# Kernel optimization log

Measured on AMD Instinct MI355X. Metric: run time of the kernel, lower is better.

Reference implementation:

```python
import jax, jax.numpy as jnp
import numpy as np
from jax import lax

T = 16        # in_length
E = 32        # input_embedding_size_d
H = 64        # encoder_size
NG = 32       # vehicles per scene group
G = 1024      # number of scene groups
N = G * NG    # total vehicles
C = 3         # class_num

leaky = lambda x: jax.nn.leaky_relu(x, 0.1)

def _gru_final(x_seq, Wih, Whh, bih, bhh):
    # x_seq: (T, N, E). PyTorch GRU gate order: r, z, n. Returns final hidden (N, H).
    def step(h, x):
        gx = x @ Wih.T + bih
        gh = h @ Whh.T + bhh
        xr, xz, xn = jnp.split(gx, 3, axis=-1)
        hr, hz, hn = jnp.split(gh, 3, axis=-1)
        r = jax.nn.sigmoid(xr + hr)
        z = jax.nn.sigmoid(xz + hz)
        ng = jnp.tanh(xn + r * hn)
        return (1.0 - z) * ng + z * h, None
    h0 = jnp.zeros((x_seq.shape[1], Whh.shape[1]), x_seq.dtype)
    hT, _ = lax.scan(step, h0, x_seq)
    return hT

def setup_inputs() -> dict:
    key = jax.random.key(0)
    ks = jax.random.split(key, 24)
    def rn(k, shape, fan):
        return jax.random.normal(k, shape, jnp.float32) * np.float32(1.0 / np.sqrt(fan))
    inp = {}
    inp["scene"] = jax.random.normal(ks[0], (N, 2 * T), jnp.float32)
    inp["condition"] = jax.random.randint(ks[1], (N,), 0, C, jnp.int32)
    inp["hero_pos_index"] = jax.random.randint(ks[2], (G,), 0, N, jnp.int32)
    inp["nbrs_pos_index"] = jax.random.randint(ks[3], (N,), 0, N, jnp.int32)
    inp["index_div"] = jnp.arange(N, dtype=jnp.int32).reshape(G, NG)
    # ip_emb_d: Linear(2, E)
    inp["W_emb"] = rn(ks[4], (2, E), 2)
    inp["b_emb"] = jnp.zeros((E,), jnp.float32)
    # forward / backward GRUs (weight_ih: (3H,E), weight_hh: (3H,H))
    inp["Wih_f"] = rn(ks[5], (3 * H, E), E); inp["Whh_f"] = rn(ks[6], (3 * H, H), H)
    inp["bih_f"] = jnp.zeros((3 * H,), jnp.float32); inp["bhh_f"] = jnp.zeros((3 * H,), jnp.float32)
    inp["Wih_b"] = rn(ks[7], (3 * H, E), E); inp["Whh_b"] = rn(ks[8], (3 * H, H), H)
    inp["bih_b"] = jnp.zeros((3 * H,), jnp.float32); inp["bhh_b"] = jnp.zeros((3 * H,), jnp.float32)
    # mlp: Linear(H, H//2)
    inp["Wm"] = rn(ks[9], (H, H // 2), H); inp["bm"] = jnp.zeros((H // 2,), jnp.float32)
    # spatial_mlp: Linear(2T, H) -> Linear(H, H//2)
    inp["Ws1"] = rn(ks[10], (2 * T, H), 2 * T); inp["bs1"] = jnp.zeros((H,), jnp.float32)
    inp["Ws2"] = rn(ks[11], (H, H // 2), H); inp["bs2"] = jnp.zeros((H // 2,), jnp.float32)
    # op_d: Linear(H, H//4) -> Linear(H//4, C)
    inp["Wo1"] = rn(ks[12], (H, H // 4), H); inp["bo1"] = jnp.zeros((H // 4,), jnp.float32)
    inp["Wo2"] = rn(ks[13], (H // 4, C), H // 4); inp["bo2"] = jnp.zeros((C,), jnp.float32)
    return inp

def reference(scene, condition, hero_pos_index, nbrs_pos_index, index_div,
              W_emb, b_emb, Wih_f, Whh_f, bih_f, bhh_f, Wih_b, Whh_b, bih_b, bhh_b,
              Wm, bm, Ws1, bs1, Ws2, bs2, Wo1, bo1, Wo2, bo2):
    n_total = scene.shape[0]
    # scene.view(-1,2,T).permute(2,0,1) -> (T, N, 2)
    scene_t = scene.reshape(n_total, 2, T).transpose(2, 0, 1)
    emb = leaky(scene_t @ W_emb + b_emb)                 # (T, N, E)
    h_f = _gru_final(emb, Wih_f, Whh_f, bih_f, bhh_f)    # (N, H)
    h_b = _gru_final(emb[::-1], Wih_b, Whh_b, bih_b, bhh_b)
    seq_enc = leaky(((h_f + h_b) * 0.5) @ Wm + bm)       # (N, H//2)
    # pairwise relative features within each group: rel[g, j, i] = x_i - x_j
    feat_g = scene[index_div]                            # (G, n, 2T); row layout == permute(1,2,0).view(-1,2T)
    rel = feat_g[:, None, :, :] - feat_g[:, :, None, :]  # (G, n, n, 2T)
    enc = leaky(leaky(rel @ Ws1 + bs1) @ Ws2 + bs2)      # (G, n, n, H//2)
    # diagonal pairs (i==j) are dropped in the original; subtract mlp(0) then divide by n-1
    zero_enc = leaky(leaky(bs1) @ Ws2 + bs2)             # (H//2,)
    n_grp = index_div.shape[1]
    pooled = (enc.sum(axis=2) - zero_enc) / (n_grp - 1)  # (G, n, H//2)
    pooled = pooled.reshape(n_total, -1)                 # group-concat order == vehicle order (arange groups)
    full_enc = jnp.concatenate([seq_enc, pooled], axis=1)  # (N, H)
    x_logit = leaky(full_enc @ Wo1 + bo1) @ Wo2 + bo2      # (N, C)
    return x_logit, full_enc
```

## Files before the change

### kernel.cpp

```cpp
#include <hip/hip_runtime.h>
#include <hip/hip_bf16.h>

#define TT 16
#define EE 32
#define HH 64
#define NGRP 32
#define CC 3

typedef __attribute__((ext_vector_type(8))) short short8;
typedef __attribute__((ext_vector_type(4))) short short4v;
typedef __attribute__((ext_vector_type(4))) float floatx4;

#define MFMA16(a, b, c) __builtin_amdgcn_mfma_f32_16x16x32_bf16((a), (b), (c), 0, 0, 0)

#define RLN2 1.4426950408889634f

__device__ __forceinline__ float leakyf(float x) { return fmaxf(x, 0.1f * x); }
__device__ __forceinline__ short f2bf(float x) {
    unsigned u = __float_as_uint(x);
    return (short)((u + 0x7FFFu + ((u >> 16) & 1u)) >> 16);
}
__device__ __forceinline__ short f2bf_h(float x) {
    return (short)((__float_as_uint(x) + 0x8000u) >> 16);
}
__device__ __forceinline__ float bf2f(short s) {
    return __uint_as_float(((unsigned)(unsigned short)s) << 16);
}
__device__ __forceinline__ short8 ld8bf(const float* __restrict__ p) {
    const float4 a = *(const float4*)p;
    const float4 b = *(const float4*)(p + 4);
    short8 v;
    v[0] = f2bf(a.x); v[1] = f2bf(a.y); v[2] = f2bf(a.z); v[3] = f2bf(a.w);
    v[4] = f2bf(b.x); v[5] = f2bf(b.y); v[6] = f2bf(b.z); v[7] = f2bf(b.w);
    return v;
}
__device__ __forceinline__ short8 ld8bfs(const float* __restrict__ p, float s) {
    const float4 a = *(const float4*)p;
    const float4 b = *(const float4*)(p + 4);
    short8 v;
    v[0] = f2bf(a.x * s); v[1] = f2bf(a.y * s); v[2] = f2bf(a.z * s); v[3] = f2bf(a.w * s);
    v[4] = f2bf(b.x * s); v[5] = f2bf(b.y * s); v[6] = f2bf(b.z * s); v[7] = f2bf(b.w * s);
    return v;
}

__global__ __launch_bounds__(256, 4) void gru_dir_kernel(
    const float* __restrict__ scene, const int* __restrict__ index_div,
    const float* __restrict__ W_emb, const float* __restrict__ b_emb,
    const float* __restrict__ Wih_f, const float* __restrict__ Whh_f,
    const float* __restrict__ bih_f, const float* __restrict__ bhh_f,
    const float* __restrict__ Wih_b, const float* __restrict__ Whh_b,
    const float* __restrict__ bih_b, const float* __restrict__ bhh_b,
    short* __restrict__ hws)
{
    __shared__ float sscene[32][33];
    __shared__ __align__(16) short Hf[2 * 2 * 2 * 64 * 8];
    __shared__ __align__(16) short Xb[2 * 2 * 64 * 8];

    const int bx   = blockIdx.x;
    const int g    = bx >> 1;
    const int dir  = bx & 1;
    const int tid  = threadIdx.x;
    const int lane = tid & 63;
    const int wd   = __builtin_amdgcn_readfirstlane(tid >> 6);
    const int cc   = lane & 15;
    const int quad = lane >> 4;
    const int j    = wd * 16 + cc;
    const int ks_w = j >> 5;
    const int qa_w = (j >> 3) & 3;
    const int ii_w = j & 7;

    #pragma unroll
    for (int rep = 0; rep < 4; ++rep) {
        const int idx = tid + rep * 256;
        const int v = idx >> 5, c = idx & 31;
        const int n = index_div[g * NGRP + v];
        sscene[c][v] = scene[n * 32 + c];
    }

    const float* Wih = dir ? Wih_b : Wih_f;
    const float* Whh = dir ? Whh_b : Whh_f;
    const float* bih = dir ? bih_b : bih_f;
    const float* bhh = dir ? bhh_b : bhh_f;
    const int k0 = quad * 8;
    const float SRZ = -RLN2, SN = 2.0f * RLN2;
    const short8 Br0  = ld8bfs(Whh + (j      ) * 64 + k0,      SRZ);
    const short8 Br1  = ld8bfs(Whh + (j      ) * 64 + 32 + k0, SRZ);
    const short8 Br2  = ld8bfs(Wih + (j      ) * 32 + k0,      SRZ);
    const short8 Bz0  = ld8bfs(Whh + (j +  64) * 64 + k0,      SRZ);
    const short8 Bz1  = ld8bfs(Whh + (j +  64) * 64 + 32 + k0, SRZ);
    const short8 Bz2  = ld8bfs(Wih + (j +  64) * 32 + k0,      SRZ);
    const short8 Bhn0 = ld8bfs(Whh + (j + 128) * 64 + k0,      SN);
    const short8 Bhn1 = ld8bfs(Whh + (j + 128) * 64 + 32 + k0, SN);
    const short8 Bxn  = ld8bfs(Wih + (j + 128) * 32 + k0,      SN);
    const float vb_r  = SRZ * (bih[j] + bhh[j]);
    const float vb_z  = SRZ * (bih[j + 64] + bhh[j + 64]);
    const float vb_xn = SN * bih[j + 128];
    const float vb_hn = SN * bhh[j + 128];

    const int veh_x = tid & 31;
    const int q2    = tid >> 5;
    const int e0    = q2 * 4;
    float w0e[4], w1e[4], bbe[4];
    #pragma unroll
    for (int d = 0; d < 4; ++d) {
        w0e[d] = W_emb[e0 + d];
        w1e[d] = W_emb[EE + e0 + d];
        bbe[d] = b_emb[e0 + d];
    }
    const int xoff = ((veh_x >> 4) * 64 + (q2 >> 1) * 16 + (veh_x & 15)) * 8
                   + (q2 & 1) * 4;

    __syncthreads();

    {
        const short8 z8 = {0, 0, 0, 0, 0, 0, 0, 0};
        *(short8*)&Hf[tid * 8] = z8;
        const int t0 = dir ? (TT - 1) : 0;
        const float xs = sscene[t0][veh_x];
        const float ys = sscene[16 + t0][veh_x];
        short4v v;
        #pragma unroll
        for (int d = 0; d < 4; ++d)
            v[d] = f2bf_h(leakyf(fmaf(xs, w0e[d], fmaf(ys, w1e[d], bbe[d]))));
        *(short4v*)&Xb[xoff] = v;
    }

    float h_reg[8];
    #pragma unroll
    for (int i = 0; i < 8; ++i) h_reg[i] = 0.0f;

    __syncthreads();

    #pragma unroll 2
    for (int s = 0; s < TT; ++s) {
        const int pb = s & 1, nb = pb ^ 1;
        const short* HfD = &Hf[pb * 2048];
        short*       HfN = &Hf[nb * 2048];
        const short* XbD = &Xb[pb * 1024];
        #pragma unroll
        for (int mt = 0; mt < 2; ++mt) {
            const short8 Ah0 = *(const short8*)&HfD[((0 * 2 + mt) * 64 + lane) * 8];
            const short8 Ah1 = *(const short8*)&HfD[((1 * 2 + mt) * 64 + lane) * 8];
            const short8 Axx = *(const short8*)&XbD[(mt * 64 + lane) * 8];
            const floatx4 z4 = {0.f, 0.f, 0.f, 0.f};
            const floatx4 ar  = MFMA16(Axx, Br2, MFMA16(Ah1, Br1, MFMA16(Ah0, Br0, z4)));
            const floatx4 az  = MFMA16(Axx, Bz2, MFMA16(Ah1, Bz1, MFMA16(Ah0, Bz0, z4)));
            const floatx4 ahn = MFMA16(Ah1, Bhn1, MFMA16(Ah0, Bhn0, z4));
            const floatx4 axn = MFMA16(Axx, Bxn, z4);
            #pragma unroll
            for (int r = 0; r < 4; ++r) {
                const float rr = __builtin_amdgcn_rcpf(1.0f + __builtin_amdgcn_exp2f(ar[r] + vb_r));
                const float zz = __builtin_amdgcn_rcpf(1.0f + __builtin_amdgcn_exp2f(az[r] + vb_z));
                const float y  = fmaf(rr, ahn[r] + vb_hn, axn[r] + vb_xn);
                const float ng = fmaf(-2.0f,
                                      __builtin_amdgcn_rcpf(__builtin_amdgcn_exp2f(y) + 1.0f),
                                      1.0f);
                const float h0 = h_reg[mt * 4 + r];
                h_reg[mt * 4 + r] = fmaf(zz, h0 - ng, ng);
            }
        }
        #pragma unroll
        for (int mt = 0; mt < 2; ++mt) {
            #pragma unroll
            for (int r = 0; r < 4; ++r) {
                const int slot = qa_w * 16 + quad * 4 + r;
                HfN[((ks_w * 2 + mt) * 64 + slot) * 8 + ii_w] = f2bf_h(h_reg[mt * 4 + r]);
            }
        }
        if (s + 1 < TT) {
            const int tn = dir ? (TT - 2 - s) : (s + 1);
            const float xs = sscene[tn][veh_x];
            const float ys = sscene[16 + tn][veh_x];
            short4v v;
            #pragma unroll
            for (int d = 0; d < 4; ++d)
                v[d] = f2bf_h(leakyf(fmaf(xs, w0e[d], fmaf(ys, w1e[d], bbe[d]))));
            *(short4v*)&Xb[xoff + nb * 1024] = v;
        }
        __syncthreads();
    }
    *(short8*)&hws[(size_t)bx * 2048 + tid * 8] = *(const short8*)&Hf[tid * 8];
}

__global__ __launch_bounds__(256, 4) void tail_kernel(
    const float* __restrict__ scene, const int* __restrict__ index_div,
    const short* __restrict__ hws,
    const float* __restrict__ Wm, const float* __restrict__ bm,
    const float* __restrict__ Ws1, const float* __restrict__ bs1,
    const float* __restrict__ Ws2, const float* __restrict__ bs2,
    const float* __restrict__ Wo1, const float* __restrict__ bo1,
    const float* __restrict__ Wo2, const float* __restrict__ bo2,
    float* __restrict__ full_enc, float* __restrict__ out)
{
    __shared__ float sscene[32][33];
    __shared__ float su[NGRP][68];
    __shared__ float fe[NGRP][68];
    __shared__ float swo1[1024];
    __shared__ float szero[32];

    const int g    = blockIdx.x;
    const int tid  = threadIdx.x;
    const int lane = tid & 63;
    const int w    = __builtin_amdgcn_readfirstlane(tid >> 6);
    const int cc   = lane & 15;
    const int quad = lane >> 4;

    #pragma unroll
    for (int rep = 0; rep < 4; ++rep) {
        const int idx = tid + rep * 256;
        const int v = idx >> 5, c = idx & 31;
        const int n = index_div[g * NGRP + v];
        sscene[c][v] = scene[n * 32 + c];
    }
    *(float4*)&swo1[tid * 4] = *(const float4*)&Wo1[tid * 4];
    if (tid < 32) {
        float zs = bs2[tid];
        #pragma unroll
        for (int d = 0; d < HH; ++d) zs = fmaf(leakyf(bs1[d]), Ws2[d * 32 + tid], zs);
        szero[tid] = leakyf(zs);
    }
    __syncthreads();

    {
        const int v  = tid >> 3;
        const int d0 = (tid & 7) * 8;
        float acc[8];
        #pragma unroll
        for (int i = 0; i < 8; ++i) acc[i] = 0.0f;
        #pragma unroll
        for (int e = 0; e < EE; ++e) {
            const float f = sscene[e][v];
            const float4 w0 = *(const float4*)&Ws1[e * 64 + d0];
            const float4 w1 = *(const float4*)&Ws1[e * 64 + d0 + 4];
            acc[0] = fmaf(f, w0.x, acc[0]); acc[1] = fmaf(f, w0.y, acc[1]);
            acc[2] = fmaf(f, w0.z, acc[2]); acc[3] = fmaf(f, w0.w, acc[3]);
            acc[4] = fmaf(f, w1.x, acc[4]); acc[5] = fmaf(f, w1.y, acc[5]);
            acc[6] = fmaf(f, w1.z, acc[6]); acc[7] = fmaf(f, w1.w, acc[7]);
        }
        #pragma unroll
        for (int i = 0; i < 8; ++i) su[v][d0 + i] = acc[i];
    }

    {
        const int nt   = w >> 1;
        const int mt_e = w & 1;
        const int n_col = nt * 16 + cc;
        short8 Bm0, Bm1;
        #pragma unroll
        for (int i = 0; i < 8; ++i) {
            Bm0[i] = f2bf(Wm[(     quad * 8 + i) * 32 + n_col]);
            Bm1[i] = f2bf(Wm[(32 + quad * 8 + i) * 32 + n_col]);
        }
        short8 A0, A1;
        #pragma unroll
        for (int ks = 0; ks < 2; ++ks) {
            const short8 F = *(const short8*)&hws[(size_t)(g * 2 + 0) * 2048 + ((ks * 2 + mt_e) * 64 + lane) * 8];
            const short8 B = *(const short8*)&hws[(size_t)(g * 2 + 1) * 2048 + ((ks * 2 + mt_e) * 64 + lane) * 8];
            #pragma unroll
            for (int i = 0; i < 8; ++i) {
                const short v = f2bf(0.5f * (bf2f(F[i]) + bf2f(B[i])));
                if (ks == 0) A0[i] = v; else A1[i] = v;
            }
        }
        const floatx4 z4 = {0.f, 0.f, 0.f, 0.f};
        const floatx4 acc = MFMA16(A1, Bm1, MFMA16(A0, Bm0, z4));
        const float bmn = bm[n_col];
        #pragma unroll
        for (int r = 0; r < 4; ++r) {
            const int veh = mt_e * 16 + quad * 4 + r;
            const float sv = leakyf(acc[r] + bmn);
            const int n = index_div[g * NGRP + veh];
            full_enc[n * HH + n_col] = sv;
            fe[veh][n_col] = sv;
        }
    }

    short8 Bw00, Bw01, Bw10, Bw11;
    #pragma unroll
    for (int i = 0; i < 8; ++i) {
        Bw00[i] = f2bf(Ws2[(     quad * 8 + i) * 32 + cc]);
        Bw01[i] = f2bf(Ws2[(32 + quad * 8 + i) * 32 + cc]);
        Bw10[i] = f2bf(Ws2[(     quad * 8 + i) * 32 + 16 + cc]);
        Bw11[i] = f2bf(Ws2[(32 + quad * 8 + i) * 32 + 16 + cc]);
    }
    float bsq0[8], bsq1[8];
    #pragma unroll
    for (int i = 0; i < 8; ++i) {
        bsq0[i] = bs1[quad * 8 + i];
        bsq1[i] = bs1[32 + quad * 8 + i];
    }
    const float bs2c0 = bs2[cc], bs2c1 = bs2[16 + cc];
    __syncthreads();

    #pragma unroll 2
    for (int jj = 0; jj < 8; ++jj) {
        const int jrow = w * 8 + jj;
        float vj0[8], vj1[8];
        #pragma unroll
        for (int i = 0; i < 8; ++i) {
            vj0[i] = su[jrow][quad * 8 + i] - bsq0[i];
            vj1[i] = su[jrow][32 + quad * 8 + i] - bsq1[i];
        }
        float acc0 = 0.0f, acc1 = 0.0f;
        #pragma unroll
        for (int it = 0; it < 2; ++it) {
            const int irow = it * 16 + cc;
            const float4 p0 = *(const float4*)&su[irow][quad * 8];
            const float4 p1 = *(const float4*)&su[irow][quad * 8 + 4];
            const float4 p2 = *(const float4*)&su[irow][32 + quad * 8];
            const float4 p3 = *(const float4*)&su[irow][32 + quad * 8 + 4];
            short8 A0, A1;
            A0[0] = f2bf(leakyf(p0.x - vj0[0])); A0[1] = f2bf(leakyf(p0.y - vj0[1]));
            A0[2] = f2bf(leakyf(p0.z - vj0[2])); A0[3] = f2bf(leakyf(p0.w - vj0[3]));
            A0[4] = f2bf(leakyf(p1.x - vj0[4])); A0[5] = f2bf(leakyf(p1.y - vj0[5]));
            A0[6] = f2bf(leakyf(p1.z - vj0[6])); A0[7] = f2bf(leakyf(p1.w - vj0[7]));
            A1[0] = f2bf(leakyf(p2.x - vj1[0])); A1[1] = f2bf(leakyf(p2.y - vj1[1]));
            A1[2] = f2bf(leakyf(p2.z - vj1[2])); A1[3] = f2bf(leakyf(p2.w - vj1[3]));
            A1[4] = f2bf(leakyf(p3.x - vj1[4])); A1[5] = f2bf(leakyf(p3.y - vj1[5]));
            A1[6] = f2bf(leakyf(p3.z - vj1[6])); A1[7] = f2bf(leakyf(p3.w - vj1[7]));
            const floatx4 z4 = {0.f, 0.f, 0.f, 0.f};
            const floatx4 D0 = MFMA16(A1, Bw01, MFMA16(A0, Bw00, z4));
            const floatx4 D1 = MFMA16(A1, Bw11, MFMA16(A0, Bw10, z4));
            #pragma unroll
            for (int r = 0; r < 4; ++r) {
                acc0 += leakyf(D0[r] + bs2c0);
                acc1 += leakyf(D1[r] + bs2c1);
            }
        }
        acc0 += __shfl_xor(acc0, 16, 64); acc0 += __shfl_xor(acc0, 32, 64);
        acc1 += __shfl_xor(acc1, 16, 64); acc1 += __shfl_xor(acc1, 32, 64);
        const int n = index_div[g * NGRP + jrow];
        if (quad == 0) {
            const float pv = (acc0 - szero[cc]) * (1.0f / 31.0f);
            full_enc[n * HH + 32 + cc] = pv;
            fe[jrow][32 + cc] = pv;
        } else if (quad == 1) {
            const float pv = (acc1 - szero[16 + cc]) * (1.0f / 31.0f);
            full_enc[n * HH + 48 + cc] = pv;
            fe[jrow][48 + cc] = pv;
        }
    }
    __syncthreads();

    {
        const int veh = tid >> 3;
        const int p   = tid & 7;
        const int m0  = p * 2;
        float a0 = bo1[m0], a1 = bo1[m0 + 1];
        #pragma unroll
        for (int k = 0; k < HH; ++k) {
            const float f = fe[veh][k];
            const float2 wv = *(const float2*)&swo1[k * 16 + m0];
            a0 = fmaf(f, wv.x, a0);
            a1 = fmaf(f, wv.y, a1);
        }
        a0 = leakyf(a0); a1 = leakyf(a1);
        float l0 = fmaf(a0, Wo2[m0 * 3 + 0], a1 * Wo2[(m0 + 1) * 3 + 0]);
        float l1 = fmaf(a0, Wo2[m0 * 3 + 1], a1 * Wo2[(m0 + 1) * 3 + 1]);
        float l2 = fmaf(a0, Wo2[m0 * 3 + 2], a1 * Wo2[(m0 + 1) * 3 + 2]);
        #pragma unroll
        for (int off = 1; off < 8; off <<= 1) {
            l0 += __shfl_xor(l0, off, 64);
            l1 += __shfl_xor(l1, off, 64);
            l2 += __shfl_xor(l2, off, 64);
        }
        if (p == 0) {
            const int n = index_div[g * NGRP + veh];
            out[n * 3 + 0] = l0 + bo2[0];
            out[n * 3 + 1] = l1 + bo2[1];
            out[n * 3 + 2] = l2 + bo2[2];
        }
    }
}

extern "C" void kernel_launch(void* const* d_in, const int* in_sizes, int n_in,
                              void* d_out, int out_size, void* d_ws, size_t ws_size,
                              hipStream_t stream) {
    const float* scene     = (const float*)d_in[0];
    const int*   index_div = (const int*)d_in[4];
    const float* W_emb = (const float*)d_in[5];
    const float* b_emb = (const float*)d_in[6];
    const float* Wih_f = (const float*)d_in[7];
    const float* Whh_f = (const float*)d_in[8];
    const float* bih_f = (const float*)d_in[9];
    const float* bhh_f = (const float*)d_in[10];
    const float* Wih_b = (const float*)d_in[11];
    const float* Whh_b = (const float*)d_in[12];
    const float* bih_b = (const float*)d_in[13];
    const float* bhh_b = (const float*)d_in[14];
    const float* Wm  = (const float*)d_in[15];
    const float* bm  = (const float*)d_in[16];
    const float* Ws1 = (const float*)d_in[17];
    const float* bs1 = (const float*)d_in[18];
    const float* Ws2 = (const float*)d_in[19];
    const float* bs2 = (const float*)d_in[20];
    const float* Wo1 = (const float*)d_in[21];
    const float* bo1 = (const float*)d_in[22];
    const float* Wo2 = (const float*)d_in[23];
    const float* bo2 = (const float*)d_in[24];

    const int N = in_sizes[0] / (2 * TT);
    const int G = in_sizes[4] / NGRP;

    float* out      = (float*)d_out;
    float* full_enc = out + (size_t)N * CC;
    short* hws      = (short*)d_ws;

    gru_dir_kernel<<<dim3(2 * G), dim3(256), 0, stream>>>(
        scene, index_div, W_emb, b_emb, Wih_f, Whh_f, bih_f, bhh_f,
        Wih_b, Whh_b, bih_b, bhh_b, hws);

    tail_kernel<<<dim3(G), dim3(256), 0, stream>>>(
        scene, index_div, hws, Wm, bm, Ws1, bs1, Ws2, bs2,
        Wo1, bo1, Wo2, bo2, full_enc, out);
}
```

Measured before the change: 200.5 us.

## Fuse GRU and tail kernels via per-group atomic last-block-done counter

Merges the bidirectional GRU kernel and the tail kernel into one launch. Each pair of direction blocks writes its final hidden state to workspace, bumps a per-group atomic counter, and the second finisher runs the pooling, MLP and output head for that group. Shared memory for the two phases is overlaid with a union, and a memset of the counters is added before the launch. This removes one kernel launch and the tail's separate pass, at the cost of extra fences and atomics, a memset, and a tail that runs on only half the blocks.

```diff
diff --git a/kernel.cpp b/kernel.cpp
--- a/kernel.cpp
+++ b/kernel.cpp
@@ -43,18 +43,35 @@
     return v;
 }
 
-__global__ __launch_bounds__(256, 4) void gru_dir_kernel(
+__global__ __launch_bounds__(256, 4) void gru_fused_kernel(
     const float* __restrict__ scene, const int* __restrict__ index_div,
     const float* __restrict__ W_emb, const float* __restrict__ b_emb,
     const float* __restrict__ Wih_f, const float* __restrict__ Whh_f,
     const float* __restrict__ bih_f, const float* __restrict__ bhh_f,
     const float* __restrict__ Wih_b, const float* __restrict__ Whh_b,
     const float* __restrict__ bih_b, const float* __restrict__ bhh_b,
-    short* __restrict__ hws)
+    const float* __restrict__ Wm, const float* __restrict__ bm,
+    const float* __restrict__ Ws1, const float* __restrict__ bs1,
+    const float* __restrict__ Ws2, const float* __restrict__ bs2,
+    const float* __restrict__ Wo1, const float* __restrict__ bo1,
+    const float* __restrict__ Wo2, const float* __restrict__ bo2,
+    short* __restrict__ hws, int* __restrict__ ctr,
+    float* __restrict__ full_enc, float* __restrict__ out)
 {
     __shared__ float sscene[32][33];
-    __shared__ __align__(16) short Hf[2 * 2 * 2 * 64 * 8];
-    __shared__ __align__(16) short Xb[2 * 2 * 64 * 8];
+    __shared__ __align__(16) union SmemU {
+        struct {
+            short Hf[2 * 2 * 2 * 64 * 8];
+            short Xb[2 * 2 * 64 * 8];
+        } g;
+        struct {
+            float su[NGRP][68];
+            float fe[NGRP][68];
+            float swo1[1024];
+            float szero[32];
+        } s;
+    } sm;
+    __shared__ int s_old;
 
     const int bx   = blockIdx.x;
     const int g    = bx >> 1;
@@ -114,7 +131,7 @@
 
     {
         const short8 z8 = {0, 0, 0, 0, 0, 0, 0, 0};
-        *(short8*)&Hf[tid * 8] = z8;
+        *(short8*)&sm.g.Hf[tid * 8] = z8;
         const int t0 = dir ? (TT - 1) : 0;
         const float xs = sscene[t0][veh_x];
         const float ys = sscene[16 + t0][veh_x];
@@ -122,7 +139,7 @@
         #pragma unroll
         for (int d = 0; d < 4; ++d)
             v[d] = f2bf_h(leakyf(fmaf(xs, w0e[d], fmaf(ys, w1e[d], bbe[d]))));
-        *(short4v*)&Xb[xoff] = v;
+        *(short4v*)&sm.g.Xb[xoff] = v;
     }
 
     float h_reg[8];
@@ -134,9 +151,9 @@
     #pragma unroll 2
     for (int s = 0; s < TT; ++s) {
         const int pb = s & 1, nb = pb ^ 1;
-        const short* HfD = &Hf[pb * 2048];
-        short*       HfN = &Hf[nb * 2048];
-        const short* XbD = &Xb[pb * 1024];
+        const short* HfD = &sm.g.Hf[pb * 2048];
+        short*       HfN = &sm.g.Hf[nb * 2048];
+        const short* XbD = &sm.g.Xb[pb * 1024];
         #pragma unroll
         for (int mt = 0; mt < 2; ++mt) {
             const short8 Ah0 = *(const short8*)&HfD[((0 * 2 + mt) * 64 + lane) * 8];
@@ -175,52 +192,27 @@
             #pragma unroll
             for (int d = 0; d < 4; ++d)
                 v[d] = f2bf_h(leakyf(fmaf(xs, w0e[d], fmaf(ys, w1e[d], bbe[d]))));
-            *(short4v*)&Xb[xoff + nb * 1024] = v;
+            *(short4v*)&sm.g.Xb[xoff + nb * 1024] = v;
         }
         __syncthreads();
     }
-    *(short8*)&hws[(size_t)bx * 2048 + tid * 8] = *(const short8*)&Hf[tid * 8];
-}
-
-__global__ __launch_bounds__(256, 4) void tail_kernel(
-    const float* __restrict__ scene, const int* __restrict__ index_div,
-    const short* __restrict__ hws,
-    const float* __restrict__ Wm, const float* __restrict__ bm,
-    const float* __restrict__ Ws1, const float* __restrict__ bs1,
-    const float* __restrict__ Ws2, const float* __restrict__ bs2,
-    const float* __restrict__ Wo1, const float* __restrict__ bo1,
-    const float* __restrict__ Wo2, const float* __restrict__ bo2,
-    float* __restrict__ full_enc, float* __restrict__ out)
-{
-    __shared__ float sscene[32][33];
-    __shared__ float su[NGRP][68];
-    __shared__ float fe[NGRP][68];
-    __shared__ float swo1[1024];
-    __shared__ float szero[32];
-
-    const int g    = blockIdx.x;
-    const int tid  = threadIdx.x;
-    const int lane = tid & 63;
-    const int w    = __builtin_amdgcn_readfirstlane(tid >> 6);
-    const int cc   = lane & 15;
-    const int quad = lane >> 4;
-
-    #pragma unroll
-    for (int rep = 0; rep < 4; ++rep) {
-        const int idx = tid + rep * 256;
-        const int v = idx >> 5, c = idx & 31;
-        const int n = index_div[g * NGRP + v];
-        sscene[c][v] = scene[n * 32 + c];
-    }
-    *(float4*)&swo1[tid * 4] = *(const float4*)&Wo1[tid * 4];
+
+    *(short8*)&hws[(size_t)bx * 2048 + tid * 8] = *(const short8*)&sm.g.Hf[tid * 8];
+    __threadfence();
+    __syncthreads();
+    if (tid == 0) s_old = atomicAdd(&ctr[g], 1);
+    __syncthreads();
+    if (s_old != 1) return;
+    __threadfence();
+
+
+    *(float4*)&sm.s.swo1[tid * 4] = *(const float4*)&Wo1[tid * 4];
     if (tid < 32) {
         float zs = bs2[tid];
         #pragma unroll
         for (int d = 0; d < HH; ++d) zs = fmaf(leakyf(bs1[d]), Ws2[d * 32 + tid], zs);
-        szero[tid] = leakyf(zs);
-    }
-    __syncthreads();
-
+        sm.s.szero[tid] = leakyf(zs);
+    }
     {
         const int v  = tid >> 3;
         const int d0 = (tid & 7) * 8;
@@ -238,12 +230,12 @@
             acc[6] = fmaf(f, w1.z, acc[6]); acc[7] = fmaf(f, w1.w, acc[7]);
         }
         #pragma unroll
-        for (int i = 0; i < 8; ++i) su[v][d0 + i] = acc[i];
+        for (int i = 0; i < 8; ++i) sm.s.su[v][d0 + i] = acc[i];
     }
 
     {
-        const int nt   = w >> 1;
-        const int mt_e = w & 1;
+        const int nt   = wd >> 1;
+        const int mt_e = wd & 1;
         const int n_col = nt * 16 + cc;
         short8 Bm0, Bm1;
         #pragma unroll
@@ -271,7 +263,7 @@
             const float sv = leakyf(acc[r] + bmn);
             const int n = index_div[g * NGRP + veh];
             full_enc[n * HH + n_col] = sv;
-            fe[veh][n_col] = sv;
+            sm.s.fe[veh][n_col] = sv;
         }
     }
 
@@ -294,21 +286,21 @@
 
     #pragma unroll 2
     for (int jj = 0; jj < 8; ++jj) {
-        const int jrow = w * 8 + jj;
+        const int jrow = wd * 8 + jj;
         float vj0[8], vj1[8];
         #pragma unroll
         for (int i = 0; i < 8; ++i) {
-            vj0[i] = su[jrow][quad * 8 + i] - bsq0[i];
-            vj1[i] = su[jrow][32 + quad * 8 + i] - bsq1[i];
+            vj0[i] = sm.s.su[jrow][quad * 8 + i] - bsq0[i];
+            vj1[i] = sm.s.su[jrow][32 + quad * 8 + i] - bsq1[i];
         }
         float acc0 = 0.0f, acc1 = 0.0f;
         #pragma unroll
         for (int it = 0; it < 2; ++it) {
             const int irow = it * 16 + cc;
-            const float4 p0 = *(const float4*)&su[irow][quad * 8];
-            const float4 p1 = *(const float4*)&su[irow][quad * 8 + 4];
-            const float4 p2 = *(const float4*)&su[irow][32 + quad * 8];
-            const float4 p3 = *(const float4*)&su[irow][32 + quad * 8 + 4];
+            const float4 p0 = *(const float4*)&sm.s.su[irow][quad * 8];
+            const float4 p1 = *(const float4*)&sm.s.su[irow][quad * 8 + 4];
+            const float4 p2 = *(const float4*)&sm.s.su[irow][32 + quad * 8];
+            const float4 p3 = *(const float4*)&sm.s.su[irow][32 + quad * 8 + 4];
             short8 A0, A1;
             A0[0] = f2bf(leakyf(p0.x - vj0[0])); A0[1] = f2bf(leakyf(p0.y - vj0[1]));
             A0[2] = f2bf(leakyf(p0.z - vj0[2])); A0[3] = f2bf(leakyf(p0.w - vj0[3]));
@@ -331,13 +323,13 @@
         acc1 += __shfl_xor(acc1, 16, 64); acc1 += __shfl_xor(acc1, 32, 64);
         const int n = index_div[g * NGRP + jrow];
         if (quad == 0) {
-            const float pv = (acc0 - szero[cc]) * (1.0f / 31.0f);
+            const float pv = (acc0 - sm.s.szero[cc]) * (1.0f / 31.0f);
             full_enc[n * HH + 32 + cc] = pv;
-            fe[jrow][32 + cc] = pv;
+            sm.s.fe[jrow][32 + cc] = pv;
         } else if (quad == 1) {
-            const float pv = (acc1 - szero[16 + cc]) * (1.0f / 31.0f);
+            const float pv = (acc1 - sm.s.szero[16 + cc]) * (1.0f / 31.0f);
             full_enc[n * HH + 48 + cc] = pv;
-            fe[jrow][48 + cc] = pv;
+            sm.s.fe[jrow][48 + cc] = pv;
         }
     }
     __syncthreads();
@@ -349,8 +341,8 @@
         float a0 = bo1[m0], a1 = bo1[m0 + 1];
         #pragma unroll
         for (int k = 0; k < HH; ++k) {
-            const float f = fe[veh][k];
-            const float2 wv = *(const float2*)&swo1[k * 16 + m0];
+            const float f = sm.s.fe[veh][k];
+            const float2 wv = *(const float2*)&sm.s.swo1[k * 16 + m0];
             a0 = fmaf(f, wv.x, a0);
             a1 = fmaf(f, wv.y, a1);
         }
@@ -405,12 +397,12 @@
     float* out      = (float*)d_out;
     float* full_enc = out + (size_t)N * CC;
     short* hws      = (short*)d_ws;
-
-    gru_dir_kernel<<<dim3(2 * G), dim3(256), 0, stream>>>(
+    int*   ctr      = (int*)((char*)d_ws + (size_t)2 * G * 2048 * sizeof(short));
+
+    hipMemsetAsync(ctr, 0, (size_t)G * sizeof(int), stream);
+
+    gru_fused_kernel<<<dim3(2 * G), dim3(256), 0, stream>>>(
         scene, index_div, W_emb, b_emb, Wih_f, Whh_f, bih_f, bhh_f,
-        Wih_b, Whh_b, bih_b, bhh_b, hws);
-
-    tail_kernel<<<dim3(G), dim3(256), 0, stream>>>(
-        scene, index_div, hws, Wm, bm, Ws1, bs1, Ws2, bs2,
-        Wo1, bo1, Wo2, bo2, full_enc, out);
-}
+        Wih_b, Whh_b, bih_b, bhh_b, Wm, bm, Ws1, bs1, Ws2, bs2,
+        Wo1, bo1, Wo2, bo2, hws, ctr, full_enc, out);
+}
```

Measured after the change: 447.5 us. +123.2%, slower.
